# Performance work log

Measured on AMD Instinct MI355X. Metric: run time of the kernel, lower is better.

The kernel has to match this reference:

```python
import jax, jax.numpy as jnp
import numpy as np
from jax import lax

C = 64
RED = 8
BN_EPS = 1e-5

def _conv1x1(x, W, b):
    # x: [N,C,H,W], W: [O,C] (1x1 conv kernel squeezed), b: [O]
    return jnp.einsum('nchw,oc->nohw', x, W) + b[None, :, None, None]

def _cross_attention(img, depth, Wq, bq, Wk, bk, Wv, bv, gamma):
    # img, depth: [N,C,H,W]; channel-channel attention (attn is [N,C,C])
    N, c, H, Wd = img.shape
    HW = H * Wd
    q = _conv1x1(img, Wq, bq).reshape(N, c, HW).astype(jnp.float32)
    k = _conv1x1(depth, Wk, bk).reshape(N, c, HW).astype(jnp.float32)
    v = _conv1x1(depth, Wv, bv).reshape(N, c, HW).astype(jnp.float32)
    attn = jax.nn.softmax(jnp.einsum('nci,ndi->ncd', q, k), axis=-1)  # [N,C,C]
    out = jnp.einsum('ncd,ndi->nci', attn, v).reshape(N, c, H, Wd).astype(img.dtype)
    return gamma * out + img

def _mlp(x, w1, b1, w2, b2):
    h = jax.nn.relu(x @ w1.T + b1)
    return h @ w2.T + b2

def _cbam(x, fc1_w, fc1_b, fc2_w, fc2_b, sa_w, sa_b):
    # x: [N,C,H,W]
    avg = x.mean(axis=(2, 3))          # [N,C]
    mx = x.max(axis=(2, 3))            # [N,C]
    ch = jax.nn.sigmoid(_mlp(avg, fc1_w, fc1_b, fc2_w, fc2_b)
                        + _mlp(mx, fc1_w, fc1_b, fc2_w, fc2_b))  # [N,C]
    x = x * ch[:, :, None, None]
    sp_in = jnp.stack([x.mean(axis=1), x.max(axis=1)], axis=1)   # [N,2,H,W]
    sp = lax.conv_general_dilated(sp_in, sa_w, (1, 1), 'SAME',
                                  dimension_numbers=('NCHW', 'OIHW', 'NCHW')) + sa_b[None, :, None, None]
    return x * jax.nn.sigmoid(sp)


def setup_inputs() -> dict:
    key = jax.random.key(0)
    ks = jax.random.split(key, 20)
    B, S, H, W = 2, 8, 128, 128
    s = 0.05
    d = {
        'img_feat': jax.random.normal(ks[0], (B, S, C, H, W), jnp.float32),
        'depth_feat': jax.random.normal(ks[1], (B, S, C, H, W), jnp.float32),
        # CrossAttention (shared module, used for both directions)
        'Wq': jax.random.normal(ks[2], (C, C), jnp.float32) * s,
        'bq': jax.random.normal(ks[3], (C,), jnp.float32) * s,
        'Wk': jax.random.normal(ks[4], (C, C), jnp.float32) * s,
        'bk': jax.random.normal(ks[5], (C,), jnp.float32) * s,
        'Wv': jax.random.normal(ks[6], (C, C), jnp.float32) * s,
        'bv': jax.random.normal(ks[7], (C,), jnp.float32) * s,
        'gamma': jax.random.normal(ks[8], (1,), jnp.float32) * 0.5,
        # fusion conv (3x3, 2C -> C) + BN (inference, running stats)
        'Wf': jax.random.normal(ks[9], (C, 2 * C, 3, 3), jnp.float32) * s,
        'bf': jax.random.normal(ks[10], (C,), jnp.float32) * s,
        'bn_g': jnp.ones((C,), jnp.float32),
        'bn_b': jnp.zeros((C,), jnp.float32),
        'bn_m': jax.random.normal(ks[11], (C,), jnp.float32) * s,
        'bn_v': jax.random.uniform(ks[12], (C,), jnp.float32, 0.5, 1.5),
        # CBAM channel MLP + spatial conv (7x7, 2 -> 1)
        'fc1_w': jax.random.normal(ks[13], (C // RED, C), jnp.float32) * s,
        'fc1_b': jax.random.normal(ks[14], (C // RED,), jnp.float32) * s,
        'fc2_w': jax.random.normal(ks[15], (C, C // RED), jnp.float32) * s,
        'fc2_b': jax.random.normal(ks[16], (C,), jnp.float32) * s,
        'sa_w': jax.random.normal(ks[17], (1, 2, 7, 7), jnp.float32) * s,
        'sa_b': jax.random.normal(ks[18], (1,), jnp.float32) * s,
    }
    return d


def reference(img_feat, depth_feat, Wq, bq, Wk, bk, Wv, bv, gamma,
              Wf, bf, bn_g, bn_b, bn_m, bn_v,
              fc1_w, fc1_b, fc2_w, fc2_b, sa_w, sa_b):
    B, S, c, H, W = img_feat.shape
    img = img_feat.reshape(-1, c, H, W)
    dep = depth_feat.reshape(-1, c, H, W)
    img_att = _cross_attention(img, dep, Wq, bq, Wk, bk, Wv, bv, gamma)
    dep_att = _cross_attention(dep, img, Wq, bq, Wk, bk, Wv, bv, gamma)
    fused = jnp.concatenate([img_att, dep_att], axis=1)  # [N,2C,H,W]
    fused = lax.conv_general_dilated(fused, Wf, (1, 1), 'SAME',
                                     dimension_numbers=('NCHW', 'OIHW', 'NCHW')) + bf[None, :, None, None]
    inv = bn_g * lax.rsqrt(bn_v + BN_EPS)
    fused = jax.nn.relu(fused * inv[None, :, None, None] + (bn_b - bn_m * inv)[None, :, None, None])
    fused = _cbam(fused, fc1_w, fc1_b, fc2_w, fc2_b, sa_w, sa_b)
    return fused.reshape(B, S, c, H, W)
```

## Files before the change

### kernel.cpp

```cpp
#include <hip/hip_runtime.h>
#include <math.h>


typedef __bf16 bf16_t;
typedef bf16_t bf16x8 __attribute__((ext_vector_type(8)));
typedef bf16_t bf16x4 __attribute__((ext_vector_type(4)));
typedef float  f32x4  __attribute__((ext_vector_type(4)));
typedef _Float16 f16_t;
typedef f16_t  f16x8  __attribute__((ext_vector_type(8)));

static constexpr int  CH  = 64;
static constexpr int  H   = 128;
static constexpr int  W   = 128;
static constexpr int  HW  = H * W;
static constexpr int  NI  = 16;
static constexpr int  NCK = 16;

static constexpr int W_WQ=0, W_BQ=4096, W_WK=4160, W_BK=8256, W_WV=8320, W_BV=12416,
  W_GAMMA=12480, W_WF=12481, W_BF=86209, W_BNG=86273, W_BNB=86337, W_BNM=86401,
  W_BNV=86465, W_FC1W=86529, W_FC1B=87041, W_FC2W=87049, W_FC2B=87561,
  W_SAW=87625, W_SAB=87723, W_TOTAL=87724;

static constexpr size_t OFF_GPART  = 0;
static constexpr size_t SZ_GPART   = (size_t)NI*NCK*4096*4;
static constexpr size_t OFF_SX     = OFF_GPART + SZ_GPART;
static constexpr size_t SZ_SXY     = (size_t)NI*NCK*64*4;
static constexpr size_t OFF_SY     = OFF_SX + SZ_SXY;
static constexpr size_t OFF_M1     = OFF_SY + SZ_SXY;
static constexpr size_t SZ_M       = (size_t)NI*4096*4;
static constexpr size_t OFF_M2     = OFF_M1 + SZ_M;
static constexpr size_t OFF_T1     = OFF_M2 + SZ_M;
static constexpr size_t SZ_T       = (size_t)NI*64*4;
static constexpr size_t OFF_T2     = OFF_T1 + SZ_T;
static constexpr size_t OFF_BCONST = OFF_T2 + SZ_T;
static constexpr size_t OFF_WH     = OFF_BCONST + 256;
static constexpr size_t SZ_WH      = (size_t)NI*64*9*128*2;
static constexpr size_t OFF_WINDT  = OFF_WH + SZ_WH;
static constexpr size_t SZ_WIND    = (size_t)NI*9*64*4;
static constexpr size_t OFF_IND    = OFF_WINDT + SZ_WIND;
static constexpr size_t OFF_BSUM   = OFF_IND + SZ_WIND;
static constexpr size_t SZ_BST     = (size_t)NI*64*64*4;
static constexpr size_t OFF_BMAX   = OFF_BSUM + SZ_BST;
static constexpr size_t OFF_CHS    = OFF_BMAX + SZ_BST;
static constexpr size_t OFF_SPIN   = OFF_CHS + SZ_T;
static constexpr size_t SZ_SPIN    = (size_t)NI*2*HW*4;
static constexpr size_t OFF_FLAG   = OFF_SPIN + SZ_SPIN;
static constexpr size_t OFF_WF32   = OFF_FLAG + 256;
static constexpr size_t OFF_P16    = ((OFF_WF32 + (size_t)W_TOTAL*4 + 255) / 256) * 256;
static constexpr size_t SZ_P16     = (size_t)NI*4*HW*32*2;

__global__ __launch_bounds__(256) void k0_detect(
    const unsigned short* __restrict__ u, int* __restrict__ flag)
{
  __shared__ int bad;
  if (threadIdx.x == 0) bad = 0;
  __syncthreads();
  int local = 0;
  for (int i = threadIdx.x; i < 4096; i += 256) {
    const unsigned short v = u[2*i];
    const int e = (v >> 7) & 0xFF;
    if (e >= 0xC0) local = 1;
  }
  if (local) atomicOr(&bad, 1);
  __syncthreads();
  if (threadIdx.x == 0) flag[0] = bad;
}

struct WPack { const void* p[19]; int sz[19]; int off[19]; };

__global__ __launch_bounds__(256) void kw_convert(
    WPack wp, const int* __restrict__ flag, float* __restrict__ dst)
{
  const int j = blockIdx.y;
  const int i = blockIdx.x * 256 + threadIdx.x;
  if (i >= wp.sz[j]) return;
  const int f32m = flag[0];
  float v;
  if (f32m) v = ((const float*)wp.p[j])[i];
  else      v = (float)((const bf16_t*)wp.p[j])[i];
  dst[wp.off[j] + i] = v;
}

__global__ __launch_bounds__(256) void kc_pack(
    const bf16_t* __restrict__ Xb, const bf16_t* __restrict__ Yb,
    const float* __restrict__ Xf, const float* __restrict__ Yf,
    const int* __restrict__ flag, f16_t* __restrict__ P16)
{
  const int lin = blockIdx.x * 256 + threadIdx.x;
  const int oct = lin & 3;
  const int p   = (lin >> 2) & 16383;
  const int s   = (lin >> 16) & 3;
  const int n   = lin >> 18;
  const int f32m = flag[0];
  const size_t nbase = (size_t)n * CH * HW;
  const int c0 = (s & 1) * 32 + oct * 8;
  const float*  Fsrc = (s < 2) ? Xf : Yf;
  const bf16_t* Bsrc = (s < 2) ? Xb : Yb;
  f16x8 h;
  #pragma unroll
  for (int j = 0; j < 8; ++j) {
    const size_t q = nbase + (size_t)(c0 + j) * HW + p;
    const float v = f32m ? Fsrc[q] : (float)Bsrc[q];
    h[j] = (f16_t)v;
  }
  *(f16x8*)(P16 + (size_t)lin * 8) = h;
}

__global__ __launch_bounds__(256) void k1_gram(
    const bf16_t* __restrict__ Xb, const bf16_t* __restrict__ Yb,
    const float* __restrict__ Xf, const float* __restrict__ Yf,
    const int* __restrict__ flag,
    float* __restrict__ Gpart, float* __restrict__ sxpart, float* __restrict__ sypart)
{
  const int chunk = blockIdx.x, n = blockIdx.y;
  const int t = threadIdx.x, lane = t & 63, wv = t >> 6;
  const int mrow = lane & 15, quad = lane >> 4;
  const int f32m = flag[0];
  const size_t nbase = (size_t)n * CH * HW;
  const int p0 = chunk * 1024 + wv * 256;

  f32x4 acc[4][4], acc2[4][4];
  #pragma unroll
  for (int i = 0; i < 4; ++i)
    #pragma unroll
    for (int j = 0; j < 4; ++j) {
      acc[i][j]  = (f32x4){0.f, 0.f, 0.f, 0.f};
      acc2[i][j] = (f32x4){0.f, 0.f, 0.f, 0.f};
    }
  float sxl[4] = {0.f,0.f,0.f,0.f}, syl[4] = {0.f,0.f,0.f,0.f};

  for (int kt = 0; kt < 8; ++kt) {
    const int pk = p0 + kt * 32 + quad * 8;
    if (f32m) {
      bf16x8 a[4], b[4], al[4], bl[4];
      #pragma unroll
      for (int mt = 0; mt < 4; ++mt) {
        const size_t ia = nbase + (size_t)(mt*16 + mrow) * HW + pk;
        float sa = 0.f, sb = 0.f;
        #pragma unroll
        for (int j = 0; j < 8; ++j) {
          const float va = Xf[ia + j];
          const bf16_t ha = (bf16_t)va;
          a[mt][j] = ha; al[mt][j] = (bf16_t)(va - (float)ha); sa += va;
          const float vb = Yf[ia + j];
          const bf16_t hb = (bf16_t)vb;
          b[mt][j] = hb; bl[mt][j] = (bf16_t)(vb - (float)hb); sb += vb;
        }
        sxl[mt] += sa; syl[mt] += sb;
      }
      #pragma unroll
      for (int mt = 0; mt < 4; ++mt)
        #pragma unroll
        for (int nt = 0; nt < 4; ++nt) {
          acc[mt][nt]  = __builtin_amdgcn_mfma_f32_16x16x32_bf16(a[mt],  b[nt],  acc[mt][nt],  0, 0, 0);
          acc2[mt][nt] = __builtin_amdgcn_mfma_f32_16x16x32_bf16(a[mt],  bl[nt], acc2[mt][nt], 0, 0, 0);
          acc2[mt][nt] = __builtin_amdgcn_mfma_f32_16x16x32_bf16(al[mt], b[nt],  acc2[mt][nt], 0, 0, 0);
        }
    } else {
      bf16x8 a[4], b[4];
      #pragma unroll
      for (int mt = 0; mt < 4; ++mt) {
        const size_t ia = nbase + (size_t)(mt*16 + mrow) * HW + pk;
        a[mt] = *(const bf16x8*)(Xb + ia);
        b[mt] = *(const bf16x8*)(Yb + ia);
        float sa = 0.f, sb = 0.f;
        #pragma unroll
        for (int j = 0; j < 8; ++j) { sa += (float)a[mt][j]; sb += (float)b[mt][j]; }
        sxl[mt] += sa; syl[mt] += sb;
      }
      #pragma unroll
      for (int mt = 0; mt < 4; ++mt)
        #pragma unroll
        for (int nt = 0; nt < 4; ++nt)
          acc[mt][nt] = __builtin_amdgcn_mfma_f32_16x16x32_bf16(a[mt], b[nt], acc[mt][nt], 0, 0, 0);
    }
  }

  #pragma unroll
  for (int mt = 0; mt < 4; ++mt) {
    sxl[mt] += __shfl_xor(sxl[mt], 16, 64); sxl[mt] += __shfl_xor(sxl[mt], 32, 64);
    syl[mt] += __shfl_xor(syl[mt], 16, 64); syl[mt] += __shfl_xor(syl[mt], 32, 64);
  }

  __shared__ float Gs[4096];
  __shared__ float sxs[64], sys[64];
  for (int w2 = 0; w2 < 4; ++w2) {
    if (wv == w2) {
      #pragma unroll
      for (int mt = 0; mt < 4; ++mt) {
        #pragma unroll
        for (int nt = 0; nt < 4; ++nt) {
          #pragma unroll
          for (int r = 0; r < 4; ++r) {
            const int c = mt*16 + quad*4 + r, d = nt*16 + mrow;
            const float val = acc[mt][nt][r] + acc2[mt][nt][r];
            if (w2 == 0) Gs[c*64 + d]  = val;
            else         Gs[c*64 + d] += val;
          }
        }
        if (quad == 0) {
          const int c = mt*16 + mrow;
          if (w2 == 0) { sxs[c] = sxl[mt];  sys[c] = syl[mt]; }
          else         { sxs[c] += sxl[mt]; sys[c] += syl[mt]; }
        }
      }
    }
    __syncthreads();
  }
  float* Gp = Gpart + ((size_t)n*NCK + chunk) * 4096;
  for (int i = t; i < 4096; i += 256) Gp[i] = Gs[i];
  if (t < 64)       sxpart[((size_t)n*NCK + chunk)*64 + t]        = sxs[t];
  else if (t < 128) sypart[((size_t)n*NCK + chunk)*64 + (t - 64)] = sys[t - 64];
}

__global__ __launch_bounds__(256) void k2a_attn(
    const float* __restrict__ Gpart, const float* __restrict__ sxpart, const float* __restrict__ sypart,
    const float* __restrict__ wt,
    float* __restrict__ M1, float* __restrict__ M2,
    float* __restrict__ T1, float* __restrict__ T2)
{
  const int n = blockIdx.x, t = threadIdx.x;
  __shared__ float Gs[4096], Gts[4160];
  __shared__ float P1s[4096], P2s[4096];
  __shared__ float A1s[4160], A2s[4160];
  __shared__ float sxs[64], sys[64], ux[64], uy[64], vx[64], vy[64];

  for (int i = t; i < 4096; i += 256) {
    float s = 0.f;
    for (int c2 = 0; c2 < NCK; ++c2) s += Gpart[((size_t)n*NCK + c2)*4096 + i];
    Gs[i] = s;
    Gts[(i & 63)*65 + (i >> 6)] = s;
  }
  if (t < 64) {
    float s = 0.f; for (int c2 = 0; c2 < NCK; ++c2) s += sxpart[((size_t)n*NCK + c2)*64 + t];
    sxs[t] = s;
  } else if (t < 128) {
    const int c = t - 64;
    float s = 0.f; for (int c2 = 0; c2 < NCK; ++c2) s += sypart[((size_t)n*NCK + c2)*64 + c];
    sys[c] = s;
  }
  __syncthreads();

  for (int i = t; i < 4096; i += 256) {
    const int c = i >> 6, e = i & 63;
    float s1 = 0.f, s2 = 0.f;
    for (int a = 0; a < 64; ++a) {
      const float w = wt[W_WQ + c*64 + a];
      s1 += w * Gs[a*64 + e];
      s2 += w * Gts[a*65 + e];
    }
    P1s[i] = s1; P2s[i] = s2;
  }
  {
    const int which = t >> 6, c = t & 63;
    float s = 0.f;
    if (which == 0)      { for (int a = 0; a < 64; ++a) s += wt[W_WQ + c*64+a]*sxs[a]; ux[c] = s; }
    else if (which == 1) { for (int a = 0; a < 64; ++a) s += wt[W_WQ + c*64+a]*sys[a]; uy[c] = s; }
    else if (which == 2) { for (int a = 0; a < 64; ++a) s += wt[W_WK + c*64+a]*sxs[a]; vx[c] = s; }
    else                 { for (int a = 0; a < 64; ++a) s += wt[W_WK + c*64+a]*sys[a]; vy[c] = s; }
  }
  __syncthreads();

  for (int i = t; i < 4096; i += 256) {
    const int c = i >> 6, d = i & 63;
    float s1 = 0.f, s2 = 0.f;
    for (int e = 0; e < 64; ++e) {
      const float wk = wt[W_WK + d*64 + e];
      s1 += P1s[c*64 + e] * wk;
      s2 += P2s[c*64 + e] * wk;
    }
    const float bqc = wt[W_BQ + c], bkd = wt[W_BK + d];
    s1 += ux[c]*bkd + bqc*vy[d] + 16384.f*bqc*bkd;
    s2 += uy[c]*bkd + bqc*vx[d] + 16384.f*bqc*bkd;
    A1s[c*65 + d] = s1; A2s[c*65 + d] = s2;
  }
  __syncthreads();

  if (t < 128) {
    float* R = (t < 64) ? (A1s + (t)*65) : (A2s + (t - 64)*65);
    float m = R[0];
    for (int d = 1; d < 64; ++d) m = fmaxf(m, R[d]);
    float s = 0.f;
    for (int d = 0; d < 64; ++d) { const float e2 = expf(R[d] - m); R[d] = e2; s += e2; }
    const float inv = 1.f / s;
    for (int d = 0; d < 64; ++d) R[d] *= inv;
  }
  __syncthreads();

  for (int i = t; i < 4096; i += 256) {
    const int c = i >> 6, e = i & 63;
    float s1 = 0.f, s2 = 0.f;
    for (int d = 0; d < 64; ++d) {
      const float wv = wt[W_WV + d*64 + e];
      s1 += A1s[c*65 + d] * wv;
      s2 += A2s[c*65 + d] * wv;
    }
    M1[(size_t)n*4096 + i] = s1;
    M2[(size_t)n*4096 + i] = s2;
  }
  if (t < 64) {
    float s1 = 0.f, s2 = 0.f;
    for (int d = 0; d < 64; ++d) {
      const float b = wt[W_BV + d];
      s1 += A1s[t*65 + d] * b;
      s2 += A2s[t*65 + d] * b;
    }
    T1[n*64 + t] = s1; T2[n*64 + t] = s2;
  }
}

__global__ __launch_bounds__(256) void k2b_weff(
    const float* __restrict__ wt,
    const float* __restrict__ M1, const float* __restrict__ M2,
    const float* __restrict__ T1, const float* __restrict__ T2,
    f16_t* __restrict__ Wh, float* __restrict__ windT, float* __restrict__ bconst)
{
  const int tap = blockIdx.x, dir = blockIdx.y, n = blockIdx.z;
  const int t = threadIdx.x;
  const float g = wt[W_GAMMA];
  f16_t* Whn = Wh + (size_t)n * 64 * 9 * 128;
  const float* Mo = (dir == 0) ? (M2 + (size_t)n*4096) : (M1 + (size_t)n*4096);

  __shared__ float Wfs[8192];
  __shared__ float Ms[4096];

  #pragma unroll
  for (int i = t; i < 8192; i += 256) Wfs[i] = wt[W_WF + i*9 + tap];
  for (int i = t; i < 4096; i += 256) Ms[i] = Mo[i];
  __syncthreads();

  const int e = t & 63;
  const int coff = dir ? 0 : 64;
  const int boff = dir ? 64 : 0;
  #pragma unroll 4
  for (int it = 0; it < 16; ++it) {
    const int o = (t >> 6) + 4*it;
    const float inv = wt[W_BNG + o] * rsqrtf(wt[W_BNV + o] + 1e-5f);
    const float base = Wfs[o*128 + boff + e];
    float s = 0.f;
    #pragma unroll 8
    for (int c = 0; c < 64; ++c)
      s += Wfs[o*128 + coff + c] * Ms[c*64 + e];
    Whn[(o*9 + tap)*128 + dir*64 + e] = (f16_t)(inv * (base + g * s));
  }

  if (dir == 0 && t < 64) {
    const int o = t;
    const float inv = wt[W_BNG + o] * rsqrtf(wt[W_BNV + o] + 1e-5f);
    float s = 0.f;
    for (int c = 0; c < 64; ++c)
      s += wt[W_WF + (o*128 + c)*9 + tap]      * T1[n*64 + c]
         + wt[W_WF + (o*128 + 64 + c)*9 + tap] * T2[n*64 + c];
    windT[((size_t)n*9 + tap)*64 + o] = inv * g * s;
    if (tap == 0 && n == 0)
      bconst[o] = wt[W_BF + o]*inv + wt[W_BNB + o] - wt[W_BNM + o]*inv;
  }
}

__global__ __launch_bounds__(64) void k2c_ind(
    const float* __restrict__ windT, float* __restrict__ ind)
{
  const int n = blockIdx.x, o = threadIdx.x;
  float w9[9];
  #pragma unroll
  for (int tp = 0; tp < 9; ++tp) w9[tp] = windT[((size_t)n*9 + tp)*64 + o];
  #pragma unroll
  for (int yc = 0; yc < 3; ++yc) {
    const int ky0 = (yc == 0) ? 1 : 0, ky1 = (yc == 2) ? 1 : 2;
    #pragma unroll
    for (int xc = 0; xc < 3; ++xc) {
      const int kx0 = (xc == 0) ? 1 : 0, kx1 = (xc == 2) ? 1 : 2;
      float s = 0.f;
      for (int ky = ky0; ky <= ky1; ++ky)
        for (int kx = kx0; kx <= kx1; ++kx) s += w9[ky*3 + kx];
      ind[((size_t)n*9 + yc*3 + xc)*64 + o] = s;
    }
  }
}

__global__ __launch_bounds__(256) void k3_conv(
    const bf16_t* __restrict__ Xb, const bf16_t* __restrict__ Yb,
    const float* __restrict__ Xf, const float* __restrict__ Yf,
    const int* __restrict__ flag,
    const f16_t* __restrict__ Wh, const float* __restrict__ bconst,
    const float* __restrict__ ind,
    const f16_t* __restrict__ P16, const int useP16,
    bf16_t* __restrict__ fusedB, float* __restrict__ fusedF,
    float* __restrict__ bsum, float* __restrict__ bmax)
{
  __shared__ __attribute__((aligned(16))) f16_t sbuf[4][130][40];
  __shared__ float sind[576], sconst[64];
  __shared__ float ssum[4][64], smax[4][64];
  const int rp = blockIdx.x, n = blockIdx.y;
  const int t = threadIdx.x, lane = t & 63, wv = t >> 6;
  const int l15 = lane & 15, quad = lane >> 4;
  const int ly = wv >> 1, ch2 = wv & 1;
  const int f32m = flag[0];
  const size_t nbase = (size_t)n * CH * HW;
  const f16_t* __restrict__ Whn = Wh + (size_t)n * 64 * 9 * 128;

  for (int i = t; i < 576; i += 256) sind[i] = ind[(size_t)n*576 + i];
  if (t < 64) sconst[t] = bconst[t];
  {
    const int r = t >> 6, cs = (t >> 5) & 1, sl = t & 31;
    sbuf[r][cs ? 129 : 0][sl] = (f16_t)0.f;
  }

  f32x4 acc[4][4];
  #pragma unroll
  for (int i = 0; i < 4; ++i)
    #pragma unroll
    for (int j = 0; j < 4; ++j) acc[i][j] = (f32x4){0.f, 0.f, 0.f, 0.f};

  const int cstage = t & 127, rsel = t >> 7;

  for (int s = 0; s < 4; ++s) {
    __syncthreads();
    if (useP16) {
      const f16_t* __restrict__ Pn = P16 + (size_t)(n*4 + s) * HW * 32;
      #pragma unroll
      for (int i = 0; i < 8; ++i) {
        const int oi  = i * 256 + t;
        const int oct = oi & 3;
        const int x   = (oi >> 2) & 127;
        const int r   = oi >> 9;
        const int gy  = rp*2 - 1 + r;
        f16x8 h;
        #pragma unroll
        for (int k = 0; k < 8; ++k) h[k] = (f16_t)0.f;
        if (gy >= 0 && gy < H)
          h = *(const f16x8*)(Pn + ((size_t)(gy*128 + x) * 32 + oct*8));
        const int colL = x + 1;
        *(f16x8*)&sbuf[r][colL][(oct ^ (colL & 3)) * 8] = h;
      }
    } else {
      #pragma unroll
      for (int pass = 0; pass < 2; ++pass) {
        const int r = rsel + 2*pass;
        const int gy = rp*2 - 1 + r;
        const bool valid = (gy >= 0) && (gy < H);
        const int colL = cstage + 1;
        #pragma unroll
        for (int oct = 0; oct < 4; ++oct) {
          f16x8 h;
          #pragma unroll
          for (int j = 0; j < 8; ++j) {
            const int g = s*32 + oct*8 + j;
            float v = 0.f;
            if (valid) {
              const size_t q = nbase + (size_t)(g & 63)*HW + gy*W + cstage;
              v = (g < 64) ? (f32m ? Xf[q] : (float)Xb[q])
                           : (f32m ? Yf[q] : (float)Yb[q]);
            }
            h[j] = (f16_t)v;
          }
          *(f16x8*)&sbuf[r][colL][(oct ^ (colL & 3)) * 8] = h;
        }
      }
    }
    __syncthreads();

    #pragma unroll
    for (int tap = 0; tap < 9; ++tap) {
      const int ky = tap / 3, kx = tap % 3;
      f16x8 bfr[4];
      #pragma unroll
      for (int nt = 0; nt < 4; ++nt) {
        const int o = nt*16 + l15;
        bfr[nt] = *(const f16x8*)(Whn + ((o*9 + tap)*128 + s*32 + quad*8));
      }
      f16x8 afr[4];
      const int row = ly + ky;
      #pragma unroll
      for (int mt = 0; mt < 4; ++mt) {
        const int col = ch2*64 + mt*16 + l15 + kx;
        afr[mt] = *(const f16x8*)&sbuf[row][col][(quad ^ (col & 3)) * 8];
      }
      #pragma unroll
      for (int mt = 0; mt < 4; ++mt)
        #pragma unroll
        for (int nt = 0; nt < 4; ++nt)
          acc[mt][nt] = __builtin_amdgcn_mfma_f32_16x16x32_f16(afr[mt], bfr[nt], acc[mt][nt], 0, 0, 0);
    }
  }

  const int y = rp*2 + ly;
  const int yc = (y == 0) ? 0 : (y == H-1) ? 2 : 1;
  #pragma unroll
  for (int nt = 0; nt < 4; ++nt) {
    const int o = nt*16 + l15;
    const float bc = sconst[o];
    float ssm = 0.f, smx = 0.f;
    #pragma unroll
    for (int mt = 0; mt < 4; ++mt) {
      const int xb = ch2*64 + mt*16 + quad*4;
      f32x4 vals;
      #pragma unroll
      for (int r = 0; r < 4; ++r) {
        const int x = xb + r;
        const int xc = (x == 0) ? 0 : (x == W-1) ? 2 : 1;
        float v = acc[mt][nt][r] + bc + sind[(yc*3 + xc)*64 + o];
        v = fmaxf(v, 0.f);
        vals[r] = v; ssm += v; smx = fmaxf(smx, v);
      }
      const size_t off = nbase + (size_t)o*HW + y*W + xb;
      if (f32m) {
        *(f32x4*)(fusedF + off) = vals;
      } else {
        bf16x4 pv;
        #pragma unroll
        for (int r = 0; r < 4; ++r) pv[r] = (bf16_t)vals[r];
        *(bf16x4*)(fusedB + off) = pv;
      }
    }
    ssm += __shfl_xor(ssm, 16, 64); ssm += __shfl_xor(ssm, 32, 64);
    smx = fmaxf(smx, __shfl_xor(smx, 16, 64));
    smx = fmaxf(smx, __shfl_xor(smx, 32, 64));
    if (quad == 0) { ssum[wv][o] = ssm; smax[wv][o] = smx; }
  }
  __syncthreads();
  if (t < 64) {
    const float S = ssum[0][t] + ssum[1][t] + ssum[2][t] + ssum[3][t];
    const float M = fmaxf(fmaxf(smax[0][t], smax[1][t]), fmaxf(smax[2][t], smax[3][t]));
    bsum[((size_t)n*64 + rp)*64 + t] = S;
    bmax[((size_t)n*64 + rp)*64 + t] = M;
  }
}

__global__ __launch_bounds__(64) void k4_chgate(
    const float* __restrict__ bsum, const float* __restrict__ bmax,
    const float* __restrict__ wt, float* __restrict__ chout)
{
  const int n = blockIdx.x, t = threadIdx.x;
  __shared__ float avg[64], mxs[64], h1[8], h2[8];
  float S = 0.f, M = 0.f;
  for (int rp = 0; rp < 64; ++rp) {
    S += bsum[((size_t)n*64 + rp)*64 + t];
    M = fmaxf(M, bmax[((size_t)n*64 + rp)*64 + t]);
  }
  avg[t] = S * (1.f / 16384.f);
  mxs[t] = M;
  __syncthreads();
  if (t < 8) {
    float s = wt[W_FC1B + t];
    for (int c = 0; c < 64; ++c) s += wt[W_FC1W + t*64 + c] * avg[c];
    h1[t] = fmaxf(s, 0.f);
  } else if (t < 16) {
    const int r = t - 8;
    float s = wt[W_FC1B + r];
    for (int c = 0; c < 64; ++c) s += wt[W_FC1W + r*64 + c] * mxs[c];
    h2[r] = fmaxf(s, 0.f);
  }
  __syncthreads();
  float s = 2.f * wt[W_FC2B + t];
  for (int r = 0; r < 8; ++r) s += wt[W_FC2W + t*8 + r] * (h1[r] + h2[r]);
  chout[n*64 + t] = 1.f / (1.f + expf(-s));
}

__global__ __launch_bounds__(256) void k5_spin(
    const bf16_t* __restrict__ fusedB, const float* __restrict__ fusedF,
    const int* __restrict__ flag,
    const float* __restrict__ chs, float* __restrict__ spin)
{
  const int n = blockIdx.y;
  const int p0 = (blockIdx.x * 256 + threadIdx.x) * 8;
  const int f32m = flag[0];
  const size_t nbase = (size_t)n * CH * HW;
  const float* c = chs + n * 64;
  float s[8], m[8];
  #pragma unroll
  for (int k = 0; k < 8; ++k) { s[k] = 0.f; m[k] = 0.f; }
  if (f32m) {
    for (int o = 0; o < 64; ++o) {
      const float co = c[o];
      const float* q = fusedF + nbase + (size_t)o*HW + p0;
      const f32x4 a = *(const f32x4*)q;
      const f32x4 b = *(const f32x4*)(q + 4);
      #pragma unroll
      for (int k = 0; k < 4; ++k) {
        const float v0 = a[k] * co; s[k]   += v0; m[k]   = fmaxf(m[k],   v0);
        const float v1 = b[k] * co; s[4+k] += v1; m[4+k] = fmaxf(m[4+k], v1);
      }
    }
  } else {
    for (int o = 0; o < 64; ++o) {
      const float co = c[o];
      const bf16x8 a = *(const bf16x8*)(fusedB + nbase + (size_t)o*HW + p0);
      #pragma unroll
      for (int k = 0; k < 8; ++k) {
        const float v = (float)a[k] * co; s[k] += v; m[k] = fmaxf(m[k], v);
      }
    }
  }
  f32x4 o0, o1, o2, o3;
  #pragma unroll
  for (int k = 0; k < 4; ++k) {
    o0[k] = s[k]   * (1.f / 64.f);
    o1[k] = s[4+k] * (1.f / 64.f);
    o2[k] = m[k];
    o3[k] = m[4+k];
  }
  *(f32x4*)(spin + (size_t)n*2*HW + p0)          = o0;
  *(f32x4*)(spin + (size_t)n*2*HW + p0 + 4)      = o1;
  *(f32x4*)(spin + (size_t)n*2*HW + HW + p0)     = o2;
  *(f32x4*)(spin + (size_t)n*2*HW + HW + p0 + 4) = o3;
}

__global__ __launch_bounds__(256) void k6_final(
    bf16_t* __restrict__ fusedB, float* __restrict__ fusedF,
    const int* __restrict__ flag,
    const float* __restrict__ chs, const float* __restrict__ spin,
    const float* __restrict__ wt)
{
  const int n = blockIdx.y;
  const int p0 = (blockIdx.x * 256 + threadIdx.x) * 8;
  const int y = p0 >> 7, x0 = p0 & 127;
  const int f32m = flag[0];
  const float* s0 = spin + (size_t)n*2*HW;
  const float* s1 = s0 + HW;
  float acc[8];
  {
    const float sab = wt[W_SAB];
    #pragma unroll
    for (int k = 0; k < 8; ++k) acc[k] = sab;
  }
  for (int j = 0; j < 7; ++j) {
    const int yy = y + j - 3;
    if (yy < 0 || yy >= H) continue;
    const float* r0 = s0 + yy*W;
    const float* r1 = s1 + yy*W;
    float v0[14], v1[14];
    #pragma unroll
    for (int ii = 0; ii < 14; ++ii) {
      const int xx = x0 + ii - 3;
      const bool ok = (xx >= 0) && (xx < W);
      v0[ii] = ok ? r0[xx] : 0.f;
      v1[ii] = ok ? r1[xx] : 0.f;
    }
    #pragma unroll
    for (int i = 0; i < 7; ++i) {
      const float w0 = wt[W_SAW + j*7 + i];
      const float w1 = wt[W_SAW + 49 + j*7 + i];
      #pragma unroll
      for (int k = 0; k < 8; ++k)
        acc[k] += w0 * v0[i+k] + w1 * v1[i+k];
    }
  }
  float sp[8];
  #pragma unroll
  for (int k = 0; k < 8; ++k) sp[k] = 1.f / (1.f + expf(-acc[k]));
  const size_t nbase = (size_t)n * CH * HW;
  const float* c = chs + n * 64;
  if (f32m) {
    for (int o = 0; o < 64; ++o) {
      const float co = c[o];
      float* q = fusedF + nbase + (size_t)o*HW + p0;
      f32x4 a = *(f32x4*)q;
      f32x4 b = *(f32x4*)(q + 4);
      #pragma unroll
      for (int k = 0; k < 4; ++k) {
        a[k] = a[k] * co * sp[k];
        b[k] = b[k] * co * sp[4+k];
      }
      *(f32x4*)q       = a;
      *(f32x4*)(q + 4) = b;
    }
  } else {
    for (int o = 0; o < 64; ++o) {
      const float co = c[o];
      bf16_t* q = fusedB + nbase + (size_t)o*HW + p0;
      bf16x8 a = *(bf16x8*)q;
      #pragma unroll
      for (int k = 0; k < 8; ++k)
        a[k] = (bf16_t)((float)a[k] * co * sp[k]);
      *(bf16x8*)q = a;
    }
  }
}

extern "C" void kernel_launch(void* const* d_in, const int* in_sizes, int n_in,
                              void* d_out, int out_size, void* d_ws, size_t ws_size,
                              hipStream_t stream)
{
  (void)n_in; (void)out_size; (void)in_sizes;
  char* ws = (char*)d_ws;
  float*  Gpart  = (float*)(ws + OFF_GPART);
  float*  sxp    = (float*)(ws + OFF_SX);
  float*  syp    = (float*)(ws + OFF_SY);
  float*  M1     = (float*)(ws + OFF_M1);
  float*  M2     = (float*)(ws + OFF_M2);
  float*  T1     = (float*)(ws + OFF_T1);
  float*  T2     = (float*)(ws + OFF_T2);
  float*  bconst = (float*)(ws + OFF_BCONST);
  f16_t*  Wh     = (f16_t*)(ws + OFF_WH);
  float*  windT  = (float*)(ws + OFF_WINDT);
  float*  indt   = (float*)(ws + OFF_IND);
  float*  bsum   = (float*)(ws + OFF_BSUM);
  float*  bmax   = (float*)(ws + OFF_BMAX);
  float*  chs    = (float*)(ws + OFF_CHS);
  float*  spin   = (float*)(ws + OFF_SPIN);
  int*    flag   = (int*)  (ws + OFF_FLAG);
  float*  wf32   = (float*)(ws + OFF_WF32);
  f16_t*  P16    = (f16_t*)(ws + OFF_P16);
  bf16_t* fusedB = (bf16_t*)d_out;
  float*  fusedF = (float*)d_out;

  const int useP16 = (ws_size >= OFF_P16 + SZ_P16) ? 1 : 0;

  const bf16_t* imgB = (const bf16_t*)d_in[0];
  const bf16_t* depB = (const bf16_t*)d_in[1];
  const float*  imgF = (const float*) d_in[0];
  const float*  depF = (const float*) d_in[1];

  WPack wp;
  static const int wsz[19] = {4096,64,4096,64,4096,64,1,73728,64,64,64,64,64,512,8,512,64,98,1};
  static const int woff[19] = {W_WQ,W_BQ,W_WK,W_BK,W_WV,W_BV,W_GAMMA,W_WF,W_BF,W_BNG,
                               W_BNB,W_BNM,W_BNV,W_FC1W,W_FC1B,W_FC2W,W_FC2B,W_SAW,W_SAB};
  for (int j = 0; j < 19; ++j) { wp.p[j] = d_in[2 + j]; wp.sz[j] = wsz[j]; wp.off[j] = woff[j]; }

  hipLaunchKernelGGL(k0_detect, dim3(1), dim3(256), 0, stream,
                     (const unsigned short*)d_in[0], flag);
  hipLaunchKernelGGL(kw_convert, dim3(288, 19), dim3(256), 0, stream, wp, flag, wf32);
  if (useP16)
    hipLaunchKernelGGL(kc_pack, dim3(16384), dim3(256), 0, stream,
                       imgB, depB, imgF, depF, flag, P16);
  hipLaunchKernelGGL(k1_gram,  dim3(NCK, NI), dim3(256), 0, stream,
                     imgB, depB, imgF, depF, flag, Gpart, sxp, syp);
  hipLaunchKernelGGL(k2a_attn, dim3(NI), dim3(256), 0, stream,
                     Gpart, sxp, syp, wf32, M1, M2, T1, T2);
  hipLaunchKernelGGL(k2b_weff, dim3(9, 2, NI), dim3(256), 0, stream,
                     wf32, M1, M2, T1, T2, Wh, windT, bconst);
  hipLaunchKernelGGL(k2c_ind,  dim3(NI), dim3(64), 0, stream, windT, indt);
  hipLaunchKernelGGL(k3_conv,  dim3(64, NI), dim3(256), 0, stream,
                     imgB, depB, imgF, depF, flag, Wh, bconst, indt,
                     P16, useP16, fusedB, fusedF, bsum, bmax);
  hipLaunchKernelGGL(k4_chgate, dim3(NI), dim3(64), 0, stream,
                     bsum, bmax, wf32, chs);
  hipLaunchKernelGGL(k5_spin,  dim3(8, NI), dim3(256), 0, stream,
                     fusedB, fusedF, flag, chs, spin);
  hipLaunchKernelGGL(k6_final, dim3(8, NI), dim3(256), 0, stream,
                     fusedB, fusedF, flag, chs, spin, wf32);
}
```

Before: 507.9 us.

## Prefetch next conv stage into registers and double the gram chunk count

In the fused 3x3 conv kernel's packed-f16 path, each stage's global loads are now issued into registers before the current stage's MFMA loop runs. They are written to shared memory after a barrier, so global latency overlaps compute. MFMA sections get raised wave priority, and the kernel gains a min-blocks-per-CU launch bound of 3. The Gram kernel splits each image into twice as many smaller chunks to raise parallelism, which doubles the partial-sum buffers and reduction work. The prefetch holds eight extra vector registers and the occupancy hint could force register spills.

```diff
diff --git a/kernel.cpp b/kernel.cpp
--- a/kernel.cpp
+++ b/kernel.cpp
@@ -14,7 +14,7 @@
 static constexpr int  W   = 128;
 static constexpr int  HW  = H * W;
 static constexpr int  NI  = 16;
-static constexpr int  NCK = 16;
+static constexpr int  NCK = 32;
 
 static constexpr int W_WQ=0, W_BQ=4096, W_WK=4160, W_BK=8256, W_WV=8320, W_BV=12416,
   W_GAMMA=12480, W_WF=12481, W_BF=86209, W_BNG=86273, W_BNB=86337, W_BNM=86401,
@@ -117,7 +117,7 @@
   const int mrow = lane & 15, quad = lane >> 4;
   const int f32m = flag[0];
   const size_t nbase = (size_t)n * CH * HW;
-  const int p0 = chunk * 1024 + wv * 256;
+  const int p0 = chunk * 512 + wv * 128;
 
   f32x4 acc[4][4], acc2[4][4];
   #pragma unroll
@@ -129,7 +129,7 @@
     }
   float sxl[4] = {0.f,0.f,0.f,0.f}, syl[4] = {0.f,0.f,0.f,0.f};
 
-  for (int kt = 0; kt < 8; ++kt) {
+  for (int kt = 0; kt < 4; ++kt) {
     const int pk = p0 + kt * 32 + quad * 8;
     if (f32m) {
       bf16x8 a[4], b[4], al[4], bl[4];
@@ -378,7 +378,7 @@
   }
 }
 
-__global__ __launch_bounds__(256) void k3_conv(
+__global__ __launch_bounds__(256, 3) void k3_conv(
     const bf16_t* __restrict__ Xb, const bf16_t* __restrict__ Yb,
     const float* __restrict__ Xf, const float* __restrict__ Yf,
     const int* __restrict__ flag,
@@ -412,28 +412,73 @@
     #pragma unroll
     for (int j = 0; j < 4; ++j) acc[i][j] = (f32x4){0.f, 0.f, 0.f, 0.f};
 
-  const int cstage = t & 127, rsel = t >> 7;
-
-  for (int s = 0; s < 4; ++s) {
-    __syncthreads();
-    if (useP16) {
-      const f16_t* __restrict__ Pn = P16 + (size_t)(n*4 + s) * HW * 32;
-      #pragma unroll
-      for (int i = 0; i < 8; ++i) {
-        const int oi  = i * 256 + t;
-        const int oct = oi & 3;
-        const int x   = (oi >> 2) & 127;
-        const int r   = oi >> 9;
-        const int gy  = rp*2 - 1 + r;
-        f16x8 h;
-        #pragma unroll
-        for (int k = 0; k < 8; ++k) h[k] = (f16_t)0.f;
-        if (gy >= 0 && gy < H)
-          h = *(const f16x8*)(Pn + ((size_t)(gy*128 + x) * 32 + oct*8));
-        const int colL = x + 1;
-        *(f16x8*)&sbuf[r][colL][(oct ^ (colL & 3)) * 8] = h;
-      }
-    } else {
+  if (useP16) {
+    const int oct = t & 3;
+    const int sl  = t >> 2;
+    const f16_t* __restrict__ PnB = P16 + (size_t)(n*4) * HW * 32;
+    f16x8 h[8];
+
+    #define K3_STAGE_LOAD(S)                                                  \
+      { const f16_t* __restrict__ Pn = PnB + (size_t)(S) * HW * 32;           \
+        _Pragma("unroll")                                                     \
+        for (int i = 0; i < 8; ++i) {                                         \
+          const int r  = i >> 1;                                              \
+          const int x  = (i & 1) * 64 + sl;                                   \
+          const int gy = rp*2 - 1 + r;                                        \
+          f16x8 v;                                                            \
+          _Pragma("unroll")                                                   \
+          for (int k2 = 0; k2 < 8; ++k2) v[k2] = (f16_t)0.f;                  \
+          if (gy >= 0 && gy < H)                                              \
+            v = *(const f16x8*)(Pn + ((size_t)(gy*128 + x) * 32 + oct*8));    \
+          h[i] = v;                                                           \
+        } }
+    #define K3_STAGE_WRITE()                                                  \
+      { _Pragma("unroll")                                                     \
+        for (int i = 0; i < 8; ++i) {                                         \
+          const int r    = i >> 1;                                            \
+          const int colL = (i & 1) * 64 + sl + 1;                             \
+          *(f16x8*)&sbuf[r][colL][(oct ^ (colL & 3)) * 8] = h[i];             \
+        } }
+
+    K3_STAGE_LOAD(0)
+    K3_STAGE_WRITE()
+    for (int s = 0; s < 4; ++s) {
+      if (s < 3) K3_STAGE_LOAD(s + 1)
+      asm volatile("s_waitcnt lgkmcnt(0)" ::: "memory");
+      __builtin_amdgcn_s_barrier();
+      __builtin_amdgcn_s_setprio(1);
+      #pragma unroll
+      for (int tap = 0; tap < 9; ++tap) {
+        const int ky = tap / 3, kx = tap % 3;
+        f16x8 bfr[4];
+        #pragma unroll
+        for (int nt = 0; nt < 4; ++nt) {
+          const int o = nt*16 + l15;
+          bfr[nt] = *(const f16x8*)(Whn + ((o*9 + tap)*128 + s*32 + quad*8));
+        }
+        f16x8 afr[4];
+        const int row = ly + ky;
+        #pragma unroll
+        for (int mt = 0; mt < 4; ++mt) {
+          const int col = ch2*64 + mt*16 + l15 + kx;
+          afr[mt] = *(const f16x8*)&sbuf[row][col][(quad ^ (col & 3)) * 8];
+        }
+        #pragma unroll
+        for (int mt = 0; mt < 4; ++mt)
+          #pragma unroll
+          for (int nt = 0; nt < 4; ++nt)
+            acc[mt][nt] = __builtin_amdgcn_mfma_f32_16x16x32_f16(afr[mt], bfr[nt], acc[mt][nt], 0, 0, 0);
+      }
+      __builtin_amdgcn_s_setprio(0);
+      __builtin_amdgcn_s_barrier();
+      if (s < 3) K3_STAGE_WRITE()
+    }
+    #undef K3_STAGE_LOAD
+    #undef K3_STAGE_WRITE
+  } else {
+    const int cstage = t & 127, rsel = t >> 7;
+    for (int s = 0; s < 4; ++s) {
+      __syncthreads();
       #pragma unroll
       for (int pass = 0; pass < 2; ++pass) {
         const int r = rsel + 2*pass;
@@ -442,7 +487,7 @@
         const int colL = cstage + 1;
         #pragma unroll
         for (int oct = 0; oct < 4; ++oct) {
-          f16x8 h;
+          f16x8 hh;
           #pragma unroll
           for (int j = 0; j < 8; ++j) {
             const int g = s*32 + oct*8 + j;
@@ -452,35 +497,34 @@
               v = (g < 64) ? (f32m ? Xf[q] : (float)Xb[q])
                            : (f32m ? Yf[q] : (float)Yb[q]);
             }
-            h[j] = (f16_t)v;
+            hh[j] = (f16_t)v;
           }
-          *(f16x8*)&sbuf[r][colL][(oct ^ (colL & 3)) * 8] = h;
-        }
-      }
-    }
-    __syncthreads();
-
-    #pragma unroll
-    for (int tap = 0; tap < 9; ++tap) {
-      const int ky = tap / 3, kx = tap % 3;
-      f16x8 bfr[4];
-      #pragma unroll
-      for (int nt = 0; nt < 4; ++nt) {
-        const int o = nt*16 + l15;
-        bfr[nt] = *(const f16x8*)(Whn + ((o*9 + tap)*128 + s*32 + quad*8));
-      }
-      f16x8 afr[4];
-      const int row = ly + ky;
-      #pragma unroll
-      for (int mt = 0; mt < 4; ++mt) {
-        const int col = ch2*64 + mt*16 + l15 + kx;
-        afr[mt] = *(const f16x8*)&sbuf[row][col][(quad ^ (col & 3)) * 8];
-      }
-      #pragma unroll
-      for (int mt = 0; mt < 4; ++mt)
-        #pragma unroll
-        for (int nt = 0; nt < 4; ++nt)
-          acc[mt][nt] = __builtin_amdgcn_mfma_f32_16x16x32_f16(afr[mt], bfr[nt], acc[mt][nt], 0, 0, 0);
+          *(f16x8*)&sbuf[r][colL][(oct ^ (colL & 3)) * 8] = hh;
+        }
+      }
+      __syncthreads();
+      #pragma unroll
+      for (int tap = 0; tap < 9; ++tap) {
+        const int ky = tap / 3, kx = tap % 3;
+        f16x8 bfr[4];
+        #pragma unroll
+        for (int nt = 0; nt < 4; ++nt) {
+          const int o = nt*16 + l15;
+          bfr[nt] = *(const f16x8*)(Whn + ((o*9 + tap)*128 + s*32 + quad*8));
+        }
+        f16x8 afr[4];
+        const int row = ly + ky;
+        #pragma unroll
+        for (int mt = 0; mt < 4; ++mt) {
+          const int col = ch2*64 + mt*16 + l15 + kx;
+          afr[mt] = *(const f16x8*)&sbuf[row][col][(quad ^ (col & 3)) * 8];
+        }
+        #pragma unroll
+        for (int mt = 0; mt < 4; ++mt)
+          #pragma unroll
+          for (int nt = 0; nt < 4; ++nt)
+            acc[mt][nt] = __builtin_amdgcn_mfma_f32_16x16x32_f16(afr[mt], bfr[nt], acc[mt][nt], 0, 0, 0);
+      }
     }
   }
 
```

Measured after the change: 586.3 us. 15.4% more time.
